# Performance work log

Measured on AMD Instinct MI355X. Metric: run time of the kernel, lower is better.

Reference implementation:

```python
import jax, jax.numpy as jnp
import numpy as np

N_NODES = 100000
N_EDGES = 3200000
IN_DIM = 256
HID_DIM = 64
OUT_DIM = 64


def setup_inputs() -> dict:
    key = jax.random.key(0)
    k1, k2, k3, k4, k5, k6 = jax.random.split(key, 6)
    x = jax.random.normal(k1, (N_NODES, IN_DIM), dtype=jnp.float32)
    edge_index = jax.random.randint(k2, (2, N_EDGES), 0, N_NODES, dtype=jnp.int32)
    # Glorot-style init for the two GCNConv layers (PyG default: glorot weight, zero bias)
    W1 = jax.random.normal(k3, (IN_DIM, HID_DIM), dtype=jnp.float32) * (1.0 / np.sqrt(IN_DIM))
    b1 = jnp.zeros((HID_DIM,), dtype=jnp.float32)
    W2 = jax.random.normal(k4, (HID_DIM, OUT_DIM), dtype=jnp.float32) * (1.0 / np.sqrt(HID_DIM))
    b2 = jnp.zeros((OUT_DIM,), dtype=jnp.float32)
    return {"x": x, "edge_index": edge_index, "W1": W1, "b1": b1, "W2": W2, "b2": b2}


def _gcn_conv(x, src, dst, deg_inv_sqrt, W, b, n):
    # PyG GCNConv: h = x W; out_i = sum_j norm_ij * h_j + b, with symmetric norm
    h = x @ W                                   # (n, d_out) small GEMM
    norm = deg_inv_sqrt[src] * deg_inv_sqrt[dst]  # (E+n,)
    msg = norm[:, None] * h[src]                # gather (E+n, d_out)
    agg = jax.ops.segment_sum(msg, dst, num_segments=n)  # scatter-add
    return agg + b


def reference(x, edge_index, W1, b1, W2, b2):
    n = x.shape[0]
    loops = jnp.arange(n, dtype=edge_index.dtype)
    src = jnp.concatenate([edge_index[0], loops])
    dst = jnp.concatenate([edge_index[1], loops])
    # degree on destination (col) with added self-loops, weight 1.0
    deg = jax.ops.segment_sum(jnp.ones_like(dst, dtype=x.dtype), dst, num_segments=n)
    deg_inv_sqrt = jnp.where(deg > 0, jax.lax.rsqrt(deg), 0.0)
    h = jax.nn.relu(_gcn_conv(x, src, dst, deg_inv_sqrt, W1, b1, n))
    return _gcn_conv(h, src, dst, deg_inv_sqrt, W2, b2, n)
```

## Files before the change

### kernel.cpp

```cpp
#include <hip/hip_runtime.h>
#include <cstdint>
#include <cstddef>


#define BIN_SHIFT 7
#define BIN_NODES 128
#define MAX_BINS 1024
#define SUP_SHIFT 11
#define FINE_PER_SUP 16
#define NSUP_MAX 64
#define SCAP 56
#define SRC_BITS 17
#define SRC_MASK ((1 << SRC_BITS) - 1)

typedef unsigned short ushort_t;

__device__ __forceinline__ float4 bfq2f4(uint2 p) {
  float4 r;
  r.x = __uint_as_float(p.x << 16);
  r.y = __uint_as_float(p.x & 0xFFFF0000u);
  r.z = __uint_as_float(p.y << 16);
  r.w = __uint_as_float(p.y & 0xFFFF0000u);
  return r;
}
__device__ __forceinline__ unsigned f2bf(float f) {
  unsigned u = __float_as_uint(f);
  return (u + 0x7FFFu + ((u >> 16) & 1u)) >> 16;
}
__device__ __forceinline__ uint2 f42bfq(float4 f) {
  uint2 r;
  r.x = f2bf(f.x) | (f2bf(f.y) << 16);
  r.y = f2bf(f.z) | (f2bf(f.w) << 16);
  return r;
}

__global__ void zero_int(int* __restrict__ p, int n) {
  int i = blockIdx.x * blockDim.x + threadIdx.x;
  if (i < n) p[i] = 0;
}

__global__ __launch_bounds__(256) void bin_count(const int* __restrict__ dst, int E, int nbins,
                                                 int* __restrict__ binCnt) {
  __shared__ int h[MAX_BINS];
  for (int i = threadIdx.x; i < nbins; i += 256) h[i] = 0;
  __syncthreads();
  int stride = gridDim.x * 256;
  for (int e = blockIdx.x * 256 + threadIdx.x; e < E; e += stride)
    atomicAdd(&h[dst[e] >> BIN_SHIFT], 1);
  __syncthreads();
  for (int i = threadIdx.x; i < nbins; i += 256)
    if (h[i]) atomicAdd(&binCnt[i], h[i]);
}

__global__ __launch_bounds__(256) void bin_scan(const int* __restrict__ binCnt, int nbins, int E,
                                                int* __restrict__ binStart,
                                                int* __restrict__ binCursor,
                                                int* __restrict__ supCursor) {
  __shared__ int s[256];
  int t = threadIdx.x;
  int c[4];
  int sum = 0;
#pragma unroll
  for (int i = 0; i < 4; i++) {
    int idx = t * 4 + i;
    c[i] = (idx < nbins) ? binCnt[idx] : 0;
    sum += c[i];
  }
  int v = sum;
  s[t] = v;
  __syncthreads();
  for (int d = 1; d < 256; d <<= 1) {
    int add = (t >= d) ? s[t - d] : 0;
    __syncthreads();
    s[t] += add;
    __syncthreads();
  }
  int run = s[t] - v;
#pragma unroll
  for (int i = 0; i < 4; i++) {
    int idx = t * 4 + i;
    if (idx < nbins) {
      binStart[idx] = run;
      binCursor[idx] = run;
      if ((idx & (FINE_PER_SUP - 1)) == 0) supCursor[idx >> 4] = run;
      run += c[i];
    }
  }
  if (t == 0) binStart[nbins] = E;
}

__global__ __launch_bounds__(256) void super_fill(const int* __restrict__ src,
                                                  const int* __restrict__ dst, int E, int nsup,
                                                  int* __restrict__ supCursor,
                                                  unsigned* __restrict__ supbuf) {
  __shared__ unsigned stage[NSUP_MAX * SCAP];
  __shared__ int lcnt[NSUP_MAX], lbase[NSUP_MAX], lscan[NSUP_MAX + 1];
  int chunk = (E + gridDim.x - 1) / gridDim.x;
  int c0 = blockIdx.x * chunk;
  int c1 = min(E, c0 + chunk);
  for (int t0 = c0; t0 < c1; t0 += 2048) {
    int t1 = min(c1, t0 + 2048);
    if (threadIdx.x < nsup) lcnt[threadIdx.x] = 0;
    __syncthreads();
    for (int e = t0 + threadIdx.x; e < t1; e += 256) {
      int d = dst[e];
      int sb = d >> SUP_SHIFT;
      unsigned v = ((unsigned)(d & ((1 << SUP_SHIFT) - 1)) << SRC_BITS) | (unsigned)src[e];
      int idx = atomicAdd(&lcnt[sb], 1);
      if (idx < SCAP)
        stage[sb * SCAP + idx] = v;
      else {
        int g = atomicAdd(&supCursor[sb], 1);
        supbuf[g] = v;
      }
    }
    __syncthreads();
    if (threadIdx.x < nsup) {
      int c = min(lcnt[threadIdx.x], SCAP);
      lcnt[threadIdx.x] = c;
      lbase[threadIdx.x] = c ? atomicAdd(&supCursor[threadIdx.x], c) : 0;
    }
    __syncthreads();
    if (threadIdx.x == 0) {
      int r = 0;
      for (int i = 0; i < nsup; i++) {
        lscan[i] = r;
        r += lcnt[i];
      }
      lscan[nsup] = r;
    }
    __syncthreads();
    int total = lscan[nsup];
    for (int j = threadIdx.x; j < total; j += 256) {
      int lo = 0, hi = nsup;
      while (hi - lo > 1) {
        int mid = (lo + hi) >> 1;
        if (lscan[mid] <= j)
          lo = mid;
        else
          hi = mid;
      }
      int off = j - lscan[lo];
      supbuf[lbase[lo] + off] = stage[lo * SCAP + off];
    }
    __syncthreads();
  }
}

__global__ __launch_bounds__(256) void fine_fill(const unsigned* __restrict__ supbuf,
                                                 const int* __restrict__ binStart, int nbins,
                                                 int* __restrict__ binCursor,
                                                 unsigned* __restrict__ binbuf) {
  __shared__ int lcnt[FINE_PER_SUP], lbase[FINE_PER_SUP];
  int sb = blockIdx.x >> 3, p = blockIdx.x & 7;
  int seg0 = binStart[sb << 4];
  int seg1 = binStart[min((sb + 1) << 4, nbins)];
  int part = (seg1 - seg0 + 7) >> 3;
  int c0 = seg0 + p * part;
  int c1 = min(seg1, c0 + part);
  if (threadIdx.x < FINE_PER_SUP) lcnt[threadIdx.x] = 0;
  __syncthreads();
  for (int i = c0 + threadIdx.x; i < c1; i += 256) atomicAdd(&lcnt[supbuf[i] >> 24], 1);
  __syncthreads();
  if (threadIdx.x < FINE_PER_SUP) {
    int c = lcnt[threadIdx.x];
    lbase[threadIdx.x] = c ? atomicAdd(&binCursor[(sb << 4) + threadIdx.x], c) : 0;
    lcnt[threadIdx.x] = 0;
  }
  __syncthreads();
  for (int i = c0 + threadIdx.x; i < c1; i += 256) {
    unsigned v = supbuf[i];
    unsigned dls = v >> SRC_BITS;
    int f = dls >> BIN_SHIFT;
    unsigned vf = ((dls & (BIN_NODES - 1)) << SRC_BITS) | (v & SRC_MASK);
    int idx = lbase[f] + atomicAdd(&lcnt[f], 1);
    binbuf[idx] = vf;
  }
}

__global__ __launch_bounds__(256) void node_count_dis(const unsigned* __restrict__ binbuf,
                                                      const int* __restrict__ binStart, int N,
                                                      int* __restrict__ count,
                                                      float* __restrict__ dis) {
  __shared__ int cnt[BIN_NODES];
  int b = blockIdx.x;
  int nodeBase = b << BIN_SHIFT;
  if (threadIdx.x < BIN_NODES) cnt[threadIdx.x] = 0;
  __syncthreads();
  int s0 = binStart[b], s1 = binStart[b + 1];
  for (int i = s0 + threadIdx.x; i < s1; i += 256) atomicAdd(&cnt[binbuf[i] >> SRC_BITS], 1);
  __syncthreads();
  if (threadIdx.x < BIN_NODES) {
    int node = nodeBase + threadIdx.x;
    if (node < N) {
      int c = cnt[threadIdx.x];
      count[node] = c;
      dis[node] = rsqrtf((float)(c + 1));
    }
  }
}

__global__ __launch_bounds__(256) void bin_csr(const unsigned* __restrict__ binbuf,
                                               const int* __restrict__ binStart,
                                               const int* __restrict__ count, int N, int E,
                                               int* __restrict__ rowptr, int* __restrict__ col) {
  __shared__ int cur[BIN_NODES];
  __shared__ int pref[BIN_NODES];
  int b = blockIdx.x, t = threadIdx.x;
  int nodeBase = b << BIN_SHIFT;
  int c = 0;
  if (t < BIN_NODES) {
    int node = nodeBase + t;
    c = (node < N) ? count[node] : 0;
    pref[t] = c;
  }
  __syncthreads();
  for (int d = 1; d < BIN_NODES; d <<= 1) {
    int add = (t < BIN_NODES && t >= d) ? pref[t - d] : 0;
    __syncthreads();
    if (t < BIN_NODES) pref[t] += add;
    __syncthreads();
  }
  int s0 = binStart[b];
  if (t < BIN_NODES) {
    int node = nodeBase + t;
    if (node < N) {
      int ex = s0 + pref[t] - c;
      rowptr[node] = ex;
      cur[t] = ex;
    }
  }
  if (b == 0 && t == 255) rowptr[N] = E;
  __syncthreads();
  int s1 = binStart[b + 1];
  for (int i = s0 + t; i < s1; i += 256) {
    unsigned v = binbuf[i];
    int slot = atomicAdd(&cur[v >> SRC_BITS], 1);
    col[slot] = v & SRC_MASK;
  }
}

template <int K, bool ABF16>
__global__ __launch_bounds__(256, 4) void gemm64(const void* __restrict__ Av,
                                                 const float* __restrict__ W,
                                                 uint2* __restrict__ Cb, int M) {
  constexpr int CHUNK = (K > 128) ? 128 : K;
  __shared__ float4 wlds[CHUNK * 16];

  const int c0 = threadIdx.x & 15;
  const int rq = threadIdx.x >> 4;
  const int r0 = blockIdx.x * 64 + rq * 4;

  float4 acc[4];
#pragma unroll
  for (int i = 0; i < 4; i++) acc[i] = make_float4(0.f, 0.f, 0.f, 0.f);
  size_t aoff[4];
  bool ok[4];
#pragma unroll
  for (int i = 0; i < 4; i++) {
    int r = r0 + i;
    ok[i] = (r < M);
    aoff[i] = (size_t)(ok[i] ? r : (M - 1)) * K;
  }

  for (int kc = 0; kc < K; kc += CHUNK) {
    {
      const float4* W4 = (const float4*)W + (size_t)kc * 16;
      for (int i = threadIdx.x; i < CHUNK * 16; i += 256) wlds[i] = W4[i];
    }
    __syncthreads();

#pragma unroll 2
    for (int k = 0; k < CHUNK; k += 4) {
      float4 xv[4];
#pragma unroll
      for (int i = 0; i < 4; i++) {
        size_t idx = aoff[i] + kc + k;
        if (ABF16)
          xv[i] = bfq2f4(*(const uint2*)((const ushort_t*)Av + idx));
        else
          xv[i] = *(const float4*)((const float*)Av + idx);
      }
      float4 w0 = wlds[(k + 0) * 16 + c0];
      float4 w1 = wlds[(k + 1) * 16 + c0];
      float4 w2 = wlds[(k + 2) * 16 + c0];
      float4 w3 = wlds[(k + 3) * 16 + c0];
#pragma unroll
      for (int i = 0; i < 4; i++) {
        acc[i].x += xv[i].x * w0.x + xv[i].y * w1.x + xv[i].z * w2.x + xv[i].w * w3.x;
        acc[i].y += xv[i].x * w0.y + xv[i].y * w1.y + xv[i].z * w2.y + xv[i].w * w3.y;
        acc[i].z += xv[i].x * w0.z + xv[i].y * w1.z + xv[i].z * w2.z + xv[i].w * w3.z;
        acc[i].w += xv[i].x * w0.w + xv[i].y * w1.w + xv[i].z * w2.w + xv[i].w * w3.w;
      }
    }
    __syncthreads();
  }
#pragma unroll
  for (int i = 0; i < 4; i++)
    if (ok[i]) Cb[(size_t)(r0 + i) * 16 + c0] = f42bfq(acc[i]);
}

template <bool OUTBF>
__global__ __launch_bounds__(256) void agg_kernel(
    const uint2* __restrict__ h, const int* __restrict__ rowptr, const int* __restrict__ col,
    const float* __restrict__ dis, const float* __restrict__ bias, void* __restrict__ outv,
    int N, int relu) {
  int wid = (blockIdx.x * blockDim.x + threadIdx.x) >> 6;
  if (wid >= N) return;
  int lane = threadIdx.x & 63;
  int sub = lane & 15;
  int quarter = lane >> 4;

  int start = rowptr[wid], end = rowptr[wid + 1];
  float di = dis[wid];

  float4 a0 = make_float4(0.f, 0.f, 0.f, 0.f), a1 = a0, a2 = a0, a3 = a0;
  {
    float4 self = bfq2f4(h[(size_t)wid * 16 + sub]);
    if (quarter == 0) {
      a0.x = di * self.x;
      a0.y = di * self.y;
      a0.z = di * self.z;
      a0.w = di * self.w;
    }
  }

  for (int base = start; base < end; base += 64) {
    int e = base + lane;
    int sj = 0;
    float wj = 0.f;
    if (e < end) {
      sj = col[e];
      wj = dis[sj];
    }
    int cnt = end - base;
    if (cnt > 64) cnt = 64;
    int rounds = (cnt + 3) >> 2;
    int t = 0;
    for (; t + 4 <= rounds; t += 4) {
      int i0 = 4 * t + quarter;
      int s0 = __shfl(sj, i0), s1 = __shfl(sj, i0 + 4), s2 = __shfl(sj, i0 + 8),
          s3 = __shfl(sj, i0 + 12);
      float w0 = __shfl(wj, i0), w1 = __shfl(wj, i0 + 4), w2 = __shfl(wj, i0 + 8),
            w3 = __shfl(wj, i0 + 12);
      float4 g0 = bfq2f4(h[(size_t)s0 * 16 + sub]);
      float4 g1 = bfq2f4(h[(size_t)s1 * 16 + sub]);
      float4 g2 = bfq2f4(h[(size_t)s2 * 16 + sub]);
      float4 g3 = bfq2f4(h[(size_t)s3 * 16 + sub]);
      a0.x += w0 * g0.x; a0.y += w0 * g0.y; a0.z += w0 * g0.z; a0.w += w0 * g0.w;
      a1.x += w1 * g1.x; a1.y += w1 * g1.y; a1.z += w1 * g1.z; a1.w += w1 * g1.w;
      a2.x += w2 * g2.x; a2.y += w2 * g2.y; a2.z += w2 * g2.z; a2.w += w2 * g2.w;
      a3.x += w3 * g3.x; a3.y += w3 * g3.y; a3.z += w3 * g3.z; a3.w += w3 * g3.w;
    }
    for (; t < rounds; t++) {
      int i0 = 4 * t + quarter;
      int s0 = __shfl(sj, i0);
      float w0 = __shfl(wj, i0);
      float4 g0 = bfq2f4(h[(size_t)s0 * 16 + sub]);
      a0.x += w0 * g0.x; a0.y += w0 * g0.y; a0.z += w0 * g0.z; a0.w += w0 * g0.w;
    }
  }

  float sx = (a0.x + a1.x) + (a2.x + a3.x);
  float sy = (a0.y + a1.y) + (a2.y + a3.y);
  float sz = (a0.z + a1.z) + (a2.z + a3.z);
  float sw = (a0.w + a1.w) + (a2.w + a3.w);
  sx += __shfl_down(sx, 32); sy += __shfl_down(sy, 32);
  sz += __shfl_down(sz, 32); sw += __shfl_down(sw, 32);
  sx += __shfl_down(sx, 16); sy += __shfl_down(sy, 16);
  sz += __shfl_down(sz, 16); sw += __shfl_down(sw, 16);
  if (quarter == 0) {
    float4 bv = ((const float4*)bias)[sub];
    float4 o = make_float4(di * sx + bv.x, di * sy + bv.y, di * sz + bv.z, di * sw + bv.w);
    if (relu) {
      o.x = fmaxf(o.x, 0.f);
      o.y = fmaxf(o.y, 0.f);
      o.z = fmaxf(o.z, 0.f);
      o.w = fmaxf(o.w, 0.f);
    }
    if (OUTBF)
      ((uint2*)outv)[(size_t)wid * 16 + sub] = f42bfq(o);
    else
      ((float4*)outv)[(size_t)wid * 16 + sub] = o;
  }
}

extern "C" void kernel_launch(void* const* d_in, const int* in_sizes, int n_in,
                              void* d_out, int out_size, void* d_ws, size_t ws_size,
                              hipStream_t stream) {
  const float* x = (const float*)d_in[0];
  const int* ei = (const int*)d_in[1];
  const float* W1 = (const float*)d_in[2];
  const float* b1 = (const float*)d_in[3];
  const float* W2 = (const float*)d_in[4];
  const float* b2 = (const float*)d_in[5];

  const int IN = 256;
  const int E = in_sizes[1] / 2;
  const int N = in_sizes[0] / IN;
  const int* src = ei;
  const int* dst = ei + E;
  const int nbins = (N + BIN_NODES - 1) >> BIN_SHIFT;
  const int nsup = (N + (1 << SUP_SHIFT) - 1) >> SUP_SHIFT;

  char* ws = (char*)d_ws;
  size_t off = 0;
  auto alloc = [&](size_t bytes) -> void* {
    void* p = ws + off;
    off += (bytes + 255) & ~(size_t)255;
    return p;
  };
  int* count = (int*)alloc((size_t)N * 4);
  int* rowptr = (int*)alloc((size_t)(N + 1) * 4);
  float* dis = (float*)alloc((size_t)N * 4);
  int* binCnt = (int*)alloc(MAX_BINS * 4);
  int* binStart = (int*)alloc((MAX_BINS + 1) * 4);
  int* binCursor = (int*)alloc(MAX_BINS * 4);
  int* supCursor = (int*)alloc(NSUP_MAX * 4);
  int* col = (int*)alloc((size_t)E * 4);
  unsigned* supbuf = (unsigned*)col;
  uint2* out1 = (uint2*)alloc((size_t)N * 64 * 2);
  size_t big = ((size_t)E * 4 > (size_t)N * 128) ? (size_t)E * 4 : (size_t)N * 128;
  unsigned* binbuf = (unsigned*)alloc(big);
  uint2* h = (uint2*)binbuf;
  float* outf = (float*)d_out;

  zero_int<<<(nbins + 255) / 256, 256, 0, stream>>>(binCnt, nbins);
  bin_count<<<1024, 256, 0, stream>>>(dst, E, nbins, binCnt);
  bin_scan<<<1, 256, 0, stream>>>(binCnt, nbins, E, binStart, binCursor, supCursor);
  super_fill<<<512, 256, 0, stream>>>(src, dst, E, nsup, supCursor, supbuf);
  fine_fill<<<nsup * 8, 256, 0, stream>>>(supbuf, binStart, nbins, binCursor, binbuf);
  node_count_dis<<<nbins, 256, 0, stream>>>(binbuf, binStart, N, count, dis);
  bin_csr<<<nbins, 256, 0, stream>>>(binbuf, binStart, count, N, E, rowptr, col);

  gemm64<256, false><<<(N + 63) / 64, 256, 0, stream>>>(x, W1, h, N);
  agg_kernel<true><<<(N + 3) / 4, 256, 0, stream>>>(h, rowptr, col, dis, b1, out1, N, 1);
  gemm64<64, true><<<(N + 63) / 64, 256, 0, stream>>>(out1, W2, h, N);
  agg_kernel<false><<<(N + 3) / 4, 256, 0, stream>>>(h, rowptr, col, dis, b2, outf, N, 0);
}
```

Measured before the change: 506.5 us.

## Replace FP32 FMA GEMMs with split-bf16 MFMA matrix-core GEMMs

Replaces the scalar FP32 GEMM kernels with MFMA 16x16x32 bf16 kernels. Inputs and weights are split into high and low bf16 parts, and three (or two) MFMAs are accumulated to keep near-FP32 accuracy. A small kernel pre-transposes and splits the weights. The aim is to cut GEMM compute time, at the cost of extra MFMA work and the loss of LDS staging for weights, which are now read from global memory per wave.

```diff
diff --git a/kernel.cpp b/kernel.cpp
--- a/kernel.cpp
+++ b/kernel.cpp
@@ -14,6 +14,14 @@
 #define SRC_MASK ((1 << SRC_BITS) - 1)
 
 typedef unsigned short ushort_t;
+
+typedef __attribute__((ext_vector_type(8))) short bf16x8;
+typedef __attribute__((ext_vector_type(4))) float f32x4;
+
+union FragB {
+  uint4 u;
+  bf16x8 b;
+};
 
 __device__ __forceinline__ float4 bfq2f4(uint2 p) {
   float4 r;
@@ -240,64 +248,122 @@
   }
 }
 
+__global__ __launch_bounds__(256) void wsplit(const float* __restrict__ W1,
+                                              const float* __restrict__ W2,
+                                              ushort_t* __restrict__ wt1,
+                                              ushort_t* __restrict__ wt2) {
+  int i = blockIdx.x * 256 + threadIdx.x;
+  const float* W;
+  ushort_t* wt;
+  int K, idx;
+  if (i < 256 * 64) {
+    W = W1; wt = wt1; K = 256; idx = i;
+  } else if (i < 256 * 64 + 64 * 64) {
+    W = W2; wt = wt2; K = 64; idx = i - 256 * 64;
+  } else
+    return;
+  int n = idx & 63, k = idx >> 6;
+  float f = W[k * 64 + n];
+  unsigned u = __float_as_uint(f);
+  unsigned hb = u & 0xFFFF0000u;
+  float lo = f - __uint_as_float(hb);
+  wt[(size_t)n * K + k] = (ushort_t)(u >> 16);
+  wt[(size_t)64 * K + (size_t)n * K + k] = (ushort_t)(__float_as_uint(lo) >> 16);
+}
+
+__device__ __forceinline__ void split8(const float* __restrict__ xp, uint4& xh, uint4& xl) {
+  float f[8];
+  *(float4*)&f[0] = *(const float4*)xp;
+  *(float4*)&f[4] = *(const float4*)(xp + 4);
+  unsigned hw[4], lw[4];
+#pragma unroll
+  for (int p = 0; p < 4; p++) {
+    unsigned ua = __float_as_uint(f[2 * p]);
+    unsigned ub = __float_as_uint(f[2 * p + 1]);
+    unsigned ha = ua & 0xFFFF0000u;
+    unsigned hb = ub & 0xFFFF0000u;
+    float la = f[2 * p] - __uint_as_float(ha);
+    float lb = f[2 * p + 1] - __uint_as_float(hb);
+    hw[p] = (ua >> 16) | hb;
+    lw[p] = (__float_as_uint(la) >> 16) | (__float_as_uint(lb) & 0xFFFF0000u);
+  }
+  xh = make_uint4(hw[0], hw[1], hw[2], hw[3]);
+  xl = make_uint4(lw[0], lw[1], lw[2], lw[3]);
+}
+
 template <int K, bool ABF16>
-__global__ __launch_bounds__(256, 4) void gemm64(const void* __restrict__ Av,
-                                                 const float* __restrict__ W,
+__global__ __launch_bounds__(256) void gemm_mfma(const void* __restrict__ Av,
+                                                 const ushort_t* __restrict__ Wt,
                                                  uint2* __restrict__ Cb, int M) {
-  constexpr int CHUNK = (K > 128) ? 128 : K;
-  __shared__ float4 wlds[CHUNK * 16];
-
-  const int c0 = threadIdx.x & 15;
-  const int rq = threadIdx.x >> 4;
-  const int r0 = blockIdx.x * 64 + rq * 4;
-
-  float4 acc[4];
-#pragma unroll
-  for (int i = 0; i < 4; i++) acc[i] = make_float4(0.f, 0.f, 0.f, 0.f);
-  size_t aoff[4];
-  bool ok[4];
-#pragma unroll
-  for (int i = 0; i < 4; i++) {
-    int r = r0 + i;
-    ok[i] = (r < M);
-    aoff[i] = (size_t)(ok[i] ? r : (M - 1)) * K;
-  }
-
-  for (int kc = 0; kc < K; kc += CHUNK) {
-    {
-      const float4* W4 = (const float4*)W + (size_t)kc * 16;
-      for (int i = threadIdx.x; i < CHUNK * 16; i += 256) wlds[i] = W4[i];
-    }
-    __syncthreads();
+  const int lane = threadIdx.x & 63;
+  const int wv = threadIdx.x >> 6;
+  const int l15 = lane & 15;
+  const int lq = lane >> 4;
+  const int m0 = blockIdx.x * 128 + wv * 32;
+
+  const ushort_t* __restrict__ Wlo = Wt + (size_t)64 * K;
+
+  f32x4 acc[2][4];
+#pragma unroll
+  for (int a = 0; a < 2; a++)
+#pragma unroll
+    for (int b = 0; b < 4; b++) acc[a][b] = (f32x4){0.f, 0.f, 0.f, 0.f};
+
+  int node[2], ncl[2];
+#pragma unroll
+  for (int mt = 0; mt < 2; mt++) {
+    node[mt] = m0 + mt * 16 + l15;
+    ncl[mt] = node[mt] < M ? node[mt] : (M - 1);
+  }
 
 #pragma unroll 2
-    for (int k = 0; k < CHUNK; k += 4) {
-      float4 xv[4];
-#pragma unroll
-      for (int i = 0; i < 4; i++) {
-        size_t idx = aoff[i] + kc + k;
-        if (ABF16)
-          xv[i] = bfq2f4(*(const uint2*)((const ushort_t*)Av + idx));
-        else
-          xv[i] = *(const float4*)((const float*)Av + idx);
+  for (int kt = 0; kt < K / 32; kt++) {
+    const int kb = kt * 32 + lq * 8;
+    FragB wh[4], wl[4];
+#pragma unroll
+    for (int nt = 0; nt < 4; nt++) {
+      wh[nt].u = *(const uint4*)(Wt + (size_t)(nt * 16 + l15) * K + kb);
+      wl[nt].u = *(const uint4*)(Wlo + (size_t)(nt * 16 + l15) * K + kb);
+    }
+#pragma unroll
+    for (int mt = 0; mt < 2; mt++) {
+      if (ABF16) {
+        FragB xa;
+        xa.u = *(const uint4*)((const ushort_t*)Av + (size_t)ncl[mt] * K + kb);
+#pragma unroll
+        for (int nt = 0; nt < 4; nt++) {
+          acc[mt][nt] =
+              __builtin_amdgcn_mfma_f32_16x16x32_bf16(wh[nt].b, xa.b, acc[mt][nt], 0, 0, 0);
+          acc[mt][nt] =
+              __builtin_amdgcn_mfma_f32_16x16x32_bf16(wl[nt].b, xa.b, acc[mt][nt], 0, 0, 0);
+        }
+      } else {
+        FragB xh, xl;
+        split8((const float*)Av + (size_t)ncl[mt] * K + kb, xh.u, xl.u);
+#pragma unroll
+        for (int nt = 0; nt < 4; nt++) {
+          acc[mt][nt] =
+              __builtin_amdgcn_mfma_f32_16x16x32_bf16(wh[nt].b, xh.b, acc[mt][nt], 0, 0, 0);
+          acc[mt][nt] =
+              __builtin_amdgcn_mfma_f32_16x16x32_bf16(wl[nt].b, xh.b, acc[mt][nt], 0, 0, 0);
+          acc[mt][nt] =
+              __builtin_amdgcn_mfma_f32_16x16x32_bf16(wh[nt].b, xl.b, acc[mt][nt], 0, 0, 0);
+        }
       }
-      float4 w0 = wlds[(k + 0) * 16 + c0];
-      float4 w1 = wlds[(k + 1) * 16 + c0];
-      float4 w2 = wlds[(k + 2) * 16 + c0];
-      float4 w3 = wlds[(k + 3) * 16 + c0];
-#pragma unroll
-      for (int i = 0; i < 4; i++) {
-        acc[i].x += xv[i].x * w0.x + xv[i].y * w1.x + xv[i].z * w2.x + xv[i].w * w3.x;
-        acc[i].y += xv[i].x * w0.y + xv[i].y * w1.y + xv[i].z * w2.y + xv[i].w * w3.y;
-        acc[i].z += xv[i].x * w0.z + xv[i].y * w1.z + xv[i].z * w2.z + xv[i].w * w3.z;
-        acc[i].w += xv[i].x * w0.w + xv[i].y * w1.w + xv[i].z * w2.w + xv[i].w * w3.w;
+    }
+  }
+
+#pragma unroll
+  for (int mt = 0; mt < 2; mt++) {
+    if (node[mt] < M) {
+      uint2* cp = Cb + (size_t)node[mt] * 16 + lq;
+#pragma unroll
+      for (int nt = 0; nt < 4; nt++) {
+        float4 o = make_float4(acc[mt][nt][0], acc[mt][nt][1], acc[mt][nt][2], acc[mt][nt][3]);
+        cp[nt * 4] = f42bfq(o);
       }
     }
-    __syncthreads();
-  }
-#pragma unroll
-  for (int i = 0; i < 4; i++)
-    if (ok[i]) Cb[(size_t)(r0 + i) * 16 + c0] = f42bfq(acc[i]);
+  }
 }
 
 template <bool OUTBF>
@@ -423,6 +489,8 @@
   size_t big = ((size_t)E * 4 > (size_t)N * 128) ? (size_t)E * 4 : (size_t)N * 128;
   unsigned* binbuf = (unsigned*)alloc(big);
   uint2* h = (uint2*)binbuf;
+  ushort_t* wt1 = (ushort_t*)alloc((size_t)2 * 64 * 256 * 2);
+  ushort_t* wt2 = (ushort_t*)alloc((size_t)2 * 64 * 64 * 2);
   float* outf = (float*)d_out;
 
   zero_int<<<(nbins + 255) / 256, 256, 0, stream>>>(binCnt, nbins);
@@ -432,9 +500,10 @@
   fine_fill<<<nsup * 8, 256, 0, stream>>>(supbuf, binStart, nbins, binCursor, binbuf);
   node_count_dis<<<nbins, 256, 0, stream>>>(binbuf, binStart, N, count, dis);
   bin_csr<<<nbins, 256, 0, stream>>>(binbuf, binStart, count, N, E, rowptr, col);
-
-  gemm64<256, false><<<(N + 63) / 64, 256, 0, stream>>>(x, W1, h, N);
+  wsplit<<<(256 * 64 + 64 * 64 + 255) / 256, 256, 0, stream>>>(W1, W2, wt1, wt2);
+
+  gemm_mfma<256, false><<<(N + 127) / 128, 256, 0, stream>>>(x, wt1, h, N);
   agg_kernel<true><<<(N + 3) / 4, 256, 0, stream>>>(h, rowptr, col, dis, b1, out1, N, 1);
-  gemm64<64, true><<<(N + 63) / 64, 256, 0, stream>>>(out1, W2, h, N);
+  gemm_mfma<64, true><<<(N + 127) / 128, 256, 0, stream>>>(out1, wt2, h, N);
   agg_kernel<false><<<(N + 3) / 4, 256, 0, stream>>>(h, rowptr, col, dis, b2, outf, N, 0);
 }
```

Result: faster. 476.6 us (-5.9%).
